# Optimization experiments

Hardware: AMD Instinct MI355X
Metric: run time of the kernel (lower is better)

Reference implementation:

```python
import jax, jax.numpy as jnp
import numpy as np
from jax import lax

DN = ('NCHW', 'OIHW', 'NCHW')


def setup_inputs() -> dict:
    key = jax.random.key(0)
    k_x, k0, k1, k2, k3 = jax.random.split(key, 5)
    return {
        'x': jax.random.normal(k_x, (16, 1, 256, 256), dtype=jnp.float32),
        'w0': jax.random.normal(k0, (16, 1, 25, 25), dtype=jnp.float32) * 0.05,
        'w1': jax.random.normal(k1, (16, 1, 49, 49), dtype=jnp.float32) * 0.02,
        'w2': jax.random.normal(k2, (16, 1, 97, 97), dtype=jnp.float32) * 0.01,
        'w3': jax.random.normal(k3, (16, 1, 193, 193), dtype=jnp.float32) * 0.005,
    }


def _energy(x, w, scale):
    # valid conv -> square -> global average pool, divided by scale. [B, 16]
    y = lax.conv_general_dilated(x, w, window_strides=(1, 1), padding='VALID',
                                 dimension_numbers=DN)
    return jnp.mean(y * y, axis=(2, 3)) / scale


def reference(x, w0, w1, w2, w3):
    feats = [
        _energy(x, w0, 1.0),
        _energy(x, w1, 2.0),
        _energy(x, w2, 4.0),
        _energy(x, w3, 8.0),
    ]
    y = jnp.stack(feats, axis=2)  # [B, 16, 4] == cat of squeezed [B,16,1] along dim 2
    y1, y2 = y[:, :8, :], y[:, 8:, :]  # split(8, dim=1)
    return y1 + y2  # [B, 8, 4]
```

## Files before the change

kernel.cpp:

```cpp
#include <hip/hip_runtime.h>
#include <hip/hip_bf16.h>

typedef __attribute__((ext_vector_type(8))) short short8v;
typedef __attribute__((ext_vector_type(4))) float f32x4;

#define IMG 256
#define NIMG 16
#define XB_ELEMS (NIMG * IMG * IMG)

#define LSTRIDE 768
#define LROWS   32
#define BBUF    (LROWS * LSTRIDE)
#define NI      (BBUF / 1024)

#define WOFF0 0u
#define WOFF1 233472u
#define WOFF2 897024u
#define WOFF3 3010560u
#define WELEMS 9461760u

__global__ void xconvert_kernel(const float* __restrict__ x,
                                __hip_bfloat16* __restrict__ xb) {
  int i = blockIdx.x * blockDim.x + threadIdx.x;
  if (i < XB_ELEMS) xb[i] = __float2bfloat16(x[i]);
}

__global__ void wpack_kernel(const float* __restrict__ w,
                             unsigned short* __restrict__ wp,
                             int K, int NSV, int total) {
  for (int idx = blockIdx.x * blockDim.x + threadIdx.x; idx < total;
       idx += gridDim.x * blockDim.x) {
    int e    = idx & 7;
    int lane = (idx >> 3) & 63;
    int rest = idx >> 9;
    int sv   = rest % NSV; rest /= NSV;
    int up   = rest % (K + 32);
    int sig  = rest / (K + 32);
    int o    = lane & 15;
    int u    = up - 16;
    int v    = sv * 32 + (lane >> 4) * 8 + e - sig;
    float val = (u >= 0 && u < K && v >= 0 && v < K) ? w[(o * K + u) * K + v] : 0.0f;
    __hip_bfloat16 h = __float2bfloat16(val);
    wp[idx] = *(unsigned short*)&h;
  }
}

template <int K, int NSV, int JBA, int WAVES, int HOUT, int IG, unsigned WOFF, int SIDX>
__device__ __forceinline__ void conv_scale(int bl,
                                           const unsigned short* __restrict__ xb,
                                           const unsigned short* __restrict__ wp,
                                           float* __restrict__ E, char* lds) {
  constexpr int RBEND = K + 16;
  constexpr int NCH   = (RBEND + 15) / 16;
  constexpr int TAIL  = RBEND - 16 * (NCH - 1);
  constexpr int M     = (NI + WAVES - 1) / WAVES;
  constexpr int WROW  = NSV * 512;
  constexpr unsigned WSLICE = (unsigned)(K + 32) * WROW;

  const int wv = threadIdx.x >> 6, lane = threadIdx.x & 63;
  const int sig = bl & 7;
  int rest = bl >> 3;
  const int ig = rest % IG, n = rest / IG;
  const int i0 = ig * 32;
  const int lr = lane & 15, lg = lane >> 4;
  const bool act = (wv < WAVES);

  const unsigned short* Wbase = wp + WOFF + (unsigned)sig * WSLICE + (unsigned)lane * 8;
  const unsigned short* Xn = xb + ((unsigned)n << 16);
  unsigned short* lds0 = (unsigned short*)lds;
  unsigned short* lds1 = (unsigned short*)(lds + BBUF);

  auto stage = [&](unsigned short* lb, int chunk) {
#pragma unroll
    for (int k2 = 0; k2 < M; ++k2) {
      int ib = wv + WAVES * k2;
      if (ib >= NI) ib = 0;
      int P = ib * 1024 + lane * 16;
      int row = P / LSTRIDE;
      int col2 = (P - row * LSTRIDE) - ((row & 7) << 4);
      int colE = col2 >> 1;
      if (colE < 0) colE = 0;
      if (colE > 248) colE = 248;
      int grow = i0 + chunk * 16 + row;
      if (grow > 255) grow = 255;
      const unsigned short* gp = Xn + (grow << 8) + colE;
      __builtin_amdgcn_global_load_lds(
          (const __attribute__((address_space(1))) unsigned int*)(const void*)gp,
          (__attribute__((address_space(3))) unsigned int*)(void*)(lb + (P >> 1)),
          16, 0, 0);
    }
  };

  f32x4 acc[2][JBA];
#pragma unroll
  for (int g = 0; g < 2; ++g)
#pragma unroll
    for (int jb = 0; jb < JBA; ++jb) acc[g][jb] = (f32x4)(0.0f);

  if (act) stage(lds0, 0);
  asm volatile("s_waitcnt vmcnt(0)" ::: "memory");
  __builtin_amdgcn_s_barrier();
  __builtin_amdgcn_sched_barrier(0);

  const int cbyte = ((wv * JBA + lg) << 4);

  for (int c = 0; c < NCH; ++c) {
    unsigned short* lb = (c & 1) ? lds1 : lds0;
    if (act) {
      if (c + 1 < NCH) stage((c & 1) ? lds0 : lds1, c + 1);
      const int RL = (c == NCH - 1) ? TAIL : 16;
      const unsigned short* Wc = Wbase + (unsigned)(c * 16) * WROW;
#pragma unroll 2
      for (int rbL = 0; rbL < RL; ++rbL) {
        const int rowLoc = rbL + lr;
        const char* abase = (const char*)lb + rowLoc * LSTRIDE +
                            ((rowLoc & 7) << 4) + cbyte;
        const unsigned short* Wr1 = Wc + rbL * WROW;
        const unsigned short* Wr0 = Wr1 + 16 * WROW;
#pragma unroll
        for (int sv = 0; sv < NSV; ++sv) {
          short8v b0 = *(const short8v*)(Wr0 + sv * 512);
          short8v b1 = *(const short8v*)(Wr1 + sv * 512);
          short8v a_[JBA];
#pragma unroll
          for (int jb = 0; jb < JBA; ++jb)
            a_[jb] = *(const short8v*)(abase + sv * 64 + jb * 16);
#pragma unroll
          for (int jb = 0; jb < JBA; ++jb) {
            acc[0][jb] = __builtin_amdgcn_mfma_f32_16x16x32_bf16(a_[jb], b0, acc[0][jb], 0, 0, 0);
            acc[1][jb] = __builtin_amdgcn_mfma_f32_16x16x32_bf16(a_[jb], b1, acc[1][jb], 0, 0, 0);
          }
        }
      }
    }
    asm volatile("s_waitcnt vmcnt(0)" ::: "memory");
    __builtin_amdgcn_sched_barrier(0);
    __builtin_amdgcn_s_barrier();
    __builtin_amdgcn_sched_barrier(0);
  }

  if (act) {
    float esum = 0.0f;
#pragma unroll
    for (int g = 0; g < 2; ++g)
#pragma unroll
      for (int jb = 0; jb < JBA; ++jb) {
        int j = sig + 8 * (wv * JBA + jb);
#pragma unroll
        for (int r2 = 0; r2 < 4; ++r2) {
          int i = i0 + 16 * g + 4 * lg + r2;
          float v = acc[g][jb][r2];
          esum += (i < HOUT && j < HOUT) ? v * v : 0.0f;
        }
      }
    esum += __shfl_xor(esum, 16, 64);
    esum += __shfl_xor(esum, 32, 64);
    if (lg == 0) atomicAdd(&E[SIDX * 256 + n * 16 + lr], esum);
  }
}

__global__ __launch_bounds__(512, 2) void conv_mfma_kernel(
    const unsigned short* __restrict__ xb, const unsigned short* __restrict__ wp,
    float* __restrict__ E) {
  extern __shared__ char lds[];
  int b = blockIdx.x;
  if (b < 256) {
    conv_scale<193, 7, 2, 4, 64, 2, WOFF3, 3>(b, xb, wp, E, lds);
  } else if (b < 896) {
    conv_scale<97, 4, 4, 5, 160, 5, WOFF2, 2>(b - 256, xb, wp, E, lds);
  } else if (b < 1792) {
    conv_scale<49, 2, 4, 7, 208, 7, WOFF1, 1>(b - 896, xb, wp, E, lds);
  } else {
    conv_scale<25, 1, 4, 8, 232, 8, WOFF0, 0>(b - 1792, xb, wp, E, lds);
  }
}

__global__ void finalize_kernel(const float* __restrict__ E, float* __restrict__ out) {
  int idx = threadIdx.x;
  if (idx >= 512) return;
  int s = idx & 3, c = (idx >> 2) & 7, n = idx >> 5;
  float denom;
  if (s == 0)      denom = 53824.0f;
  else if (s == 1) denom = 86528.0f;
  else if (s == 2) denom = 102400.0f;
  else             denom = 32768.0f;
  out[idx] = (E[s * 256 + n * 16 + c] + E[s * 256 + n * 16 + c + 8]) / denom;
}

extern "C" void kernel_launch(void* const* d_in, const int* in_sizes, int n_in,
                              void* d_out, int out_size, void* d_ws, size_t ws_size,
                              hipStream_t stream) {
  const float* x = (const float*)d_in[0];
  const float* w[4] = {(const float*)d_in[1], (const float*)d_in[2],
                       (const float*)d_in[3], (const float*)d_in[4]};
  static const int Ks[4]   = {25, 49, 97, 193};
  static const int NSVs[4] = {1, 2, 4, 7};
  static const unsigned wOff[4] = {WOFF0, WOFF1, WOFF2, WOFF3};

  char* wsb = (char*)d_ws;
  float* E = (float*)wsb;
  __hip_bfloat16* xb = (__hip_bfloat16*)(wsb + 4096);
  unsigned short* wp = (unsigned short*)(wsb + 4096 + (size_t)XB_ELEMS * 2);

  hipMemsetAsync(E, 0, 1024 * sizeof(float), stream);
  xconvert_kernel<<<(XB_ELEMS + 255) / 256, 256, 0, stream>>>(x, xb);
  for (int s = 0; s < 4; ++s) {
    int total = 8 * (Ks[s] + 32) * NSVs[s] * 512;
    wpack_kernel<<<(total + 255) / 256, 256, 0, stream>>>(w[s], wp + wOff[s],
                                                          Ks[s], NSVs[s], total);
  }
  conv_mfma_kernel<<<2816, 512, 2 * BBUF, stream>>>((const unsigned short*)xb, wp, E);
  finalize_kernel<<<1, 512, 0, stream>>>(E, (float*)d_out);
}
```

Before: 496.9 us.

## Restructure conv tiling: split kernel rows, pair shifts, producer waves, XOR-swizzled LDS

Reorganizes the MFMA convolution. Each block now handles two column shifts at once, so every A fragment read from LDS feeds twice as many MFMAs. The large kernels are split along kernel rows across two blocks. The weight packing drops the 32 rows of zero padding and the two row groups are handled by separate GM-specialized loop bodies, which removes MFMAs on zero weights. LDS shrinks to a 512-byte row stride with an XOR swizzle, occupancy rises to 4 blocks per CU, and when fewer than 8 waves compute, the idle waves act as dedicated producers that stage input tiles. The cost is more atomics, more code paths, and tighter register pressure under the higher occupancy bound.

```diff
diff --git a/kernel.cpp b/kernel.cpp
--- a/kernel.cpp
+++ b/kernel.cpp
@@ -8,16 +8,13 @@
 #define NIMG 16
 #define XB_ELEMS (NIMG * IMG * IMG)
 
-#define LSTRIDE 768
-#define LROWS   32
-#define BBUF    (LROWS * LSTRIDE)
-#define NI      (BBUF / 1024)
-
-#define WOFF0 0u
-#define WOFF1 233472u
-#define WOFF2 897024u
-#define WOFF3 3010560u
-#define WELEMS 9461760u
+#define WQ0 0u
+#define WQ1 102400u
+#define WQ2 503808u
+#define WQ3 2093056u
+#define WQEND 7624704u
+
+#define BUFB 16384
 
 __global__ void xconvert_kernel(const float* __restrict__ x,
                                 __hip_bfloat16* __restrict__ xb) {
@@ -26,152 +23,225 @@
 }
 
 __global__ void wpack_kernel(const float* __restrict__ w,
-                             unsigned short* __restrict__ wp,
+                             unsigned short* __restrict__ wq,
                              int K, int NSV, int total) {
   for (int idx = blockIdx.x * blockDim.x + threadIdx.x; idx < total;
        idx += gridDim.x * blockDim.x) {
-    int e    = idx & 7;
-    int lane = (idx >> 3) & 63;
-    int rest = idx >> 9;
-    int sv   = rest % NSV; rest /= NSV;
-    int up   = rest % (K + 32);
-    int sig  = rest / (K + 32);
-    int o    = lane & 15;
-    int u    = up - 16;
-    int v    = sv * 32 + (lane >> 4) * 8 + e - sig;
-    float val = (u >= 0 && u < K && v >= 0 && v < K) ? w[(o * K + u) * K + v] : 0.0f;
+    int e = idx & 7, lane = (idx >> 3) & 63, rest = idx >> 9;
+    int sv = rest % NSV; rest /= NSV;
+    int u = rest % K, sig = rest / K;
+    int o = lane & 15;
+    int v = sv * 32 + (lane >> 4) * 8 + e - sig;
+    float val = (v >= 0 && v < K) ? w[(o * K + u) * K + v] : 0.0f;
     __hip_bfloat16 h = __float2bfloat16(val);
-    wp[idx] = *(unsigned short*)&h;
-  }
-}
-
-template <int K, int NSV, int JBA, int WAVES, int HOUT, int IG, unsigned WOFF, int SIDX>
-__device__ __forceinline__ void conv_scale(int bl,
-                                           const unsigned short* __restrict__ xb,
-                                           const unsigned short* __restrict__ wp,
-                                           float* __restrict__ E, char* lds) {
-  constexpr int RBEND = K + 16;
-  constexpr int NCH   = (RBEND + 15) / 16;
-  constexpr int TAIL  = RBEND - 16 * (NCH - 1);
-  constexpr int M     = (NI + WAVES - 1) / WAVES;
-  constexpr int WROW  = NSV * 512;
-  constexpr unsigned WSLICE = (unsigned)(K + 32) * WROW;
+    wq[idx] = *(unsigned short*)&h;
+  }
+}
+
+template <int GM, int NSV, int JBA>
+__device__ __forceinline__ void kbody(int c, int rb0, int rb1, const char* bufc,
+                                      const unsigned short* __restrict__ Wa,
+                                      const unsigned short* __restrict__ Wb,
+                                      int cbBase, int lr, f32x4 (&acc)[2][2][JBA]) {
+#pragma unroll 1
+  for (int rbL = rb0; rbL < rb1; ++rbL) {
+    const int rowLoc = rbL + lr;
+    const char* rbase = bufc + rowLoc * 512;
+    const int u0i = 16 * c + rbL;
+#pragma unroll
+    for (int sv = 0; sv < NSV; ++sv) {
+      short8v a_[JBA];
+#pragma unroll
+      for (int jb = 0; jb < JBA; ++jb) {
+        int cb = cbBase + 16 * jb + 64 * sv;
+        int addr = (cb & ~127) + ((((cb >> 4) ^ rowLoc) & 7) << 4);
+        a_[jb] = *(const short8v*)(rbase + addr);
+      }
+      if (GM & 1) {
+        const int wo = (u0i * NSV + sv) * 512;
+        short8v ba = *(const short8v*)(Wa + wo);
+        short8v bb = *(const short8v*)(Wb + wo);
+#pragma unroll
+        for (int jb = 0; jb < JBA; ++jb) {
+          acc[0][0][jb] = __builtin_amdgcn_mfma_f32_16x16x32_bf16(a_[jb], ba, acc[0][0][jb], 0, 0, 0);
+          acc[0][1][jb] = __builtin_amdgcn_mfma_f32_16x16x32_bf16(a_[jb], bb, acc[0][1][jb], 0, 0, 0);
+        }
+      }
+      if (GM & 2) {
+        const int wo = ((u0i - 16) * NSV + sv) * 512;
+        short8v ba = *(const short8v*)(Wa + wo);
+        short8v bb = *(const short8v*)(Wb + wo);
+#pragma unroll
+        for (int jb = 0; jb < JBA; ++jb) {
+          acc[1][0][jb] = __builtin_amdgcn_mfma_f32_16x16x32_bf16(a_[jb], ba, acc[1][0][jb], 0, 0, 0);
+          acc[1][1][jb] = __builtin_amdgcn_mfma_f32_16x16x32_bf16(a_[jb], bb, acc[1][1][jb], 0, 0, 0);
+        }
+      }
+    }
+  }
+}
+
+template <int KL, int KFULL, int NSV, int JBA, int WC, int HOUT, int SIDX>
+__device__ __forceinline__ void conv_scale(const unsigned short* __restrict__ xb,
+                                           const unsigned short* __restrict__ wq_s,
+                                           float* __restrict__ E, char* lds,
+                                           int n, int i0, int u0, int q) {
+  constexpr int M16 = KL >> 4, R = KL & 15;
+  constexpr int NCH = M16 + (R ? 2 : 1);
+  constexpr unsigned SSTRIDE = (unsigned)KFULL * NSV * 512;
 
   const int wv = threadIdx.x >> 6, lane = threadIdx.x & 63;
-  const int sig = bl & 7;
-  int rest = bl >> 3;
-  const int ig = rest % IG, n = rest / IG;
-  const int i0 = ig * 32;
   const int lr = lane & 15, lg = lane >> 4;
-  const bool act = (wv < WAVES);
-
-  const unsigned short* Wbase = wp + WOFF + (unsigned)sig * WSLICE + (unsigned)lane * 8;
+  const bool isProd = (WC < 8) && (wv >= WC);
   const unsigned short* Xn = xb + ((unsigned)n << 16);
-  unsigned short* lds0 = (unsigned short*)lds;
-  unsigned short* lds1 = (unsigned short*)(lds + BBUF);
-
-  auto stage = [&](unsigned short* lb, int chunk) {
+  const int rowG0 = i0 + u0;
+
+  const unsigned short* Wa = wq_s + (unsigned)(2 * q) * SSTRIDE +
+                             (unsigned)(u0 * NSV) * 512 + lane * 8;
+  const unsigned short* Wb = Wa + SSTRIDE;
+
+  auto stage = [&](int cn) {
+    char* dst = lds + (cn & 1) * BUFB;
+    constexpr int NSTG = (WC < 8) ? (8 - WC) : 8;
+    const int sid = (WC < 8) ? (wv - WC) : wv;
+    constexpr int M = (16 + NSTG - 1) / NSTG;
 #pragma unroll
     for (int k2 = 0; k2 < M; ++k2) {
-      int ib = wv + WAVES * k2;
-      if (ib >= NI) ib = 0;
+      int ib = sid + NSTG * k2;
+      if (ib >= 16) ib = 0;
       int P = ib * 1024 + lane * 16;
-      int row = P / LSTRIDE;
-      int col2 = (P - row * LSTRIDE) - ((row & 7) << 4);
-      int colE = col2 >> 1;
-      if (colE < 0) colE = 0;
-      if (colE > 248) colE = 248;
-      int grow = i0 + chunk * 16 + row;
+      int lrow = P >> 9;
+      int slot = (P >> 4) & 31;
+      int srcslot = (slot & ~7) | ((slot ^ lrow) & 7);
+      int grow = rowG0 + cn * 16 + lrow;
       if (grow > 255) grow = 255;
-      const unsigned short* gp = Xn + (grow << 8) + colE;
+      const unsigned short* gp = Xn + (grow << 8) + srcslot * 8;
       __builtin_amdgcn_global_load_lds(
           (const __attribute__((address_space(1))) unsigned int*)(const void*)gp,
-          (__attribute__((address_space(3))) unsigned int*)(void*)(lb + (P >> 1)),
-          16, 0, 0);
+          (__attribute__((address_space(3))) unsigned int*)(void*)(dst + P), 16, 0, 0);
     }
   };
 
-  f32x4 acc[2][JBA];
+  if (isProd) {
+    stage(0);
+    asm volatile("s_waitcnt vmcnt(0)" ::: "memory");
+    __builtin_amdgcn_s_barrier();
+    for (int c = 0; c < NCH; ++c) {
+      if (c + 1 < NCH) {
+        stage(c + 1);
+        asm volatile("s_waitcnt vmcnt(0)" ::: "memory");
+      }
+      __builtin_amdgcn_s_barrier();
+    }
+    return;
+  }
+
+  f32x4 acc[2][2][JBA];
 #pragma unroll
   for (int g = 0; g < 2; ++g)
 #pragma unroll
-    for (int jb = 0; jb < JBA; ++jb) acc[g][jb] = (f32x4)(0.0f);
-
-  if (act) stage(lds0, 0);
-  asm volatile("s_waitcnt vmcnt(0)" ::: "memory");
+    for (int sj = 0; sj < 2; ++sj)
+#pragma unroll
+      for (int jb = 0; jb < JBA; ++jb) acc[g][sj][jb] = (f32x4)(0.0f);
+
+  const int t0 = wv * JBA;
+  const int cbBase = 16 * t0 + 16 * lg;
+
+  if (WC == 8) {
+    stage(0);
+    asm volatile("s_waitcnt vmcnt(0)" ::: "memory");
+  }
   __builtin_amdgcn_s_barrier();
-  __builtin_amdgcn_sched_barrier(0);
-
-  const int cbyte = ((wv * JBA + lg) << 4);
-
-  for (int c = 0; c < NCH; ++c) {
-    unsigned short* lb = (c & 1) ? lds1 : lds0;
-    if (act) {
-      if (c + 1 < NCH) stage((c & 1) ? lds0 : lds1, c + 1);
-      const int RL = (c == NCH - 1) ? TAIL : 16;
-      const unsigned short* Wc = Wbase + (unsigned)(c * 16) * WROW;
-#pragma unroll 2
-      for (int rbL = 0; rbL < RL; ++rbL) {
-        const int rowLoc = rbL + lr;
-        const char* abase = (const char*)lb + rowLoc * LSTRIDE +
-                            ((rowLoc & 7) << 4) + cbyte;
-        const unsigned short* Wr1 = Wc + rbL * WROW;
-        const unsigned short* Wr0 = Wr1 + 16 * WROW;
-#pragma unroll
-        for (int sv = 0; sv < NSV; ++sv) {
-          short8v b0 = *(const short8v*)(Wr0 + sv * 512);
-          short8v b1 = *(const short8v*)(Wr1 + sv * 512);
-          short8v a_[JBA];
-#pragma unroll
-          for (int jb = 0; jb < JBA; ++jb)
-            a_[jb] = *(const short8v*)(abase + sv * 64 + jb * 16);
-#pragma unroll
-          for (int jb = 0; jb < JBA; ++jb) {
-            acc[0][jb] = __builtin_amdgcn_mfma_f32_16x16x32_bf16(a_[jb], b0, acc[0][jb], 0, 0, 0);
-            acc[1][jb] = __builtin_amdgcn_mfma_f32_16x16x32_bf16(a_[jb], b1, acc[1][jb], 0, 0, 0);
-          }
-        }
-      }
-    }
-    asm volatile("s_waitcnt vmcnt(0)" ::: "memory");
-    __builtin_amdgcn_sched_barrier(0);
-    __builtin_amdgcn_s_barrier();
-    __builtin_amdgcn_sched_barrier(0);
-  }
-
-  if (act) {
-    float esum = 0.0f;
-#pragma unroll
-    for (int g = 0; g < 2; ++g)
+
+#define STEP_PRE(c)  if (WC == 8 && (c) + 1 < NCH) stage((c) + 1);
+#define STEP_POST()  if (WC == 8) asm volatile("s_waitcnt vmcnt(0)" ::: "memory"); \
+                     __builtin_amdgcn_s_barrier();
+
+  {
+    const char* bufc = lds;
+    STEP_PRE(0)
+    kbody<1, NSV, JBA>(0, 0, 16, bufc, Wa, Wb, cbBase, lr, acc);
+    STEP_POST()
+  }
+#pragma unroll 1
+  for (int c = 1; c < M16; ++c) {
+    const char* bufc = lds + (c & 1) * BUFB;
+    STEP_PRE(c)
+    kbody<3, NSV, JBA>(c, 0, 16, bufc, Wa, Wb, cbBase, lr, acc);
+    STEP_POST()
+  }
+  if (R > 0) {
+    {
+      const char* bufc = lds + (M16 & 1) * BUFB;
+      STEP_PRE(M16)
+      kbody<3, NSV, JBA>(M16, 0, R, bufc, Wa, Wb, cbBase, lr, acc);
+      kbody<2, NSV, JBA>(M16, R, 16, bufc, Wa, Wb, cbBase, lr, acc);
+      STEP_POST()
+    }
+    {
+      const char* bufc = lds + ((M16 + 1) & 1) * BUFB;
+      kbody<2, NSV, JBA>(M16 + 1, 0, R, bufc, Wa, Wb, cbBase, lr, acc);
+      STEP_POST()
+    }
+  } else {
+    const char* bufc = lds + (M16 & 1) * BUFB;
+    kbody<2, NSV, JBA>(M16, 0, 16, bufc, Wa, Wb, cbBase, lr, acc);
+    STEP_POST()
+  }
+#undef STEP_PRE
+#undef STEP_POST
+
+  float esum = 0.0f;
+#pragma unroll
+  for (int g = 0; g < 2; ++g)
+#pragma unroll
+    for (int sj = 0; sj < 2; ++sj)
 #pragma unroll
       for (int jb = 0; jb < JBA; ++jb) {
-        int j = sig + 8 * (wv * JBA + jb);
+        int j = 8 * (t0 + jb) + 2 * q + sj;
 #pragma unroll
         for (int r2 = 0; r2 < 4; ++r2) {
           int i = i0 + 16 * g + 4 * lg + r2;
-          float v = acc[g][jb][r2];
+          float v = acc[g][sj][jb][r2];
           esum += (i < HOUT && j < HOUT) ? v * v : 0.0f;
         }
       }
-    esum += __shfl_xor(esum, 16, 64);
-    esum += __shfl_xor(esum, 32, 64);
-    if (lg == 0) atomicAdd(&E[SIDX * 256 + n * 16 + lr], esum);
-  }
-}
-
-__global__ __launch_bounds__(512, 2) void conv_mfma_kernel(
-    const unsigned short* __restrict__ xb, const unsigned short* __restrict__ wp,
+  esum += __shfl_xor(esum, 16, 64);
+  esum += __shfl_xor(esum, 32, 64);
+  if (lg == 0) atomicAdd(&E[SIDX * 256 + n * 16 + lr], esum);
+}
+
+__global__ __launch_bounds__(512, 4) void conv_mfma_kernel(
+    const unsigned short* __restrict__ xb, const unsigned short* __restrict__ wq,
     float* __restrict__ E) {
-  extern __shared__ char lds[];
+  __shared__ char lds[2 * BUFB];
   int b = blockIdx.x;
   if (b < 256) {
-    conv_scale<193, 7, 2, 4, 64, 2, WOFF3, 3>(b, xb, wp, E, lds);
+    int q = (b & 7) >> 1;
+    int rest = ((b >> 3) << 1) | (b & 1);
+    int ks = rest & 1, ig = (rest >> 1) & 1, n = rest >> 2;
+    if (ks == 0) conv_scale<96, 193, 7, 2, 4, 64, 3>(xb, wq + WQ3, E, lds, n, ig * 32, 0, q);
+    else         conv_scale<97, 193, 7, 2, 4, 64, 3>(xb, wq + WQ3, E, lds, n, ig * 32, 96, q);
   } else if (b < 896) {
-    conv_scale<97, 4, 4, 5, 160, 5, WOFF2, 2>(b - 256, xb, wp, E, lds);
-  } else if (b < 1792) {
-    conv_scale<49, 2, 4, 7, 208, 7, WOFF1, 1>(b - 896, xb, wp, E, lds);
+    int bl = b - 256;
+    int q = (bl & 7) >> 1;
+    int rest = ((bl >> 3) << 1) | (bl & 1);
+    int ks = rest & 1, r2 = rest >> 1;
+    int ig = r2 % 5, n = r2 / 5;
+    if (ks == 0) conv_scale<48, 97, 4, 4, 5, 160, 2>(xb, wq + WQ2, E, lds, n, ig * 32, 0, q);
+    else         conv_scale<49, 97, 4, 4, 5, 160, 2>(xb, wq + WQ2, E, lds, n, ig * 32, 48, q);
+  } else if (b < 1344) {
+    int bl = b - 896;
+    int q = (bl & 7) >> 1;
+    int rest = ((bl >> 3) << 1) | (bl & 1);
+    int ig = rest % 7, n = rest / 7;
+    conv_scale<49, 49, 2, 4, 7, 208, 1>(xb, wq + WQ1, E, lds, n, ig * 32, 0, q);
   } else {
-    conv_scale<25, 1, 4, 8, 232, 8, WOFF0, 0>(b - 1792, xb, wp, E, lds);
+    int bl = b - 1344;
+    int q = (bl & 7) >> 1;
+    int rest = ((bl >> 3) << 1) | (bl & 1);
+    int ig = rest & 7, n = rest >> 3;
+    conv_scale<25, 25, 1, 4, 8, 232, 0>(xb, wq + WQ0, E, lds, n, ig * 32, 0, q);
   }
 }
 
@@ -193,22 +263,21 @@
   const float* x = (const float*)d_in[0];
   const float* w[4] = {(const float*)d_in[1], (const float*)d_in[2],
                        (const float*)d_in[3], (const float*)d_in[4]};
-  static const int Ks[4]   = {25, 49, 97, 193};
+  static const int Ks[4] = {25, 49, 97, 193};
   static const int NSVs[4] = {1, 2, 4, 7};
-  static const unsigned wOff[4] = {WOFF0, WOFF1, WOFF2, WOFF3};
+  static const unsigned wOff[4] = {WQ0, WQ1, WQ2, WQ3};
 
   char* wsb = (char*)d_ws;
   float* E = (float*)wsb;
   __hip_bfloat16* xb = (__hip_bfloat16*)(wsb + 4096);
-  unsigned short* wp = (unsigned short*)(wsb + 4096 + (size_t)XB_ELEMS * 2);
+  unsigned short* wq = (unsigned short*)(wsb + 4096 + (size_t)XB_ELEMS * 2);
 
   hipMemsetAsync(E, 0, 1024 * sizeof(float), stream);
   xconvert_kernel<<<(XB_ELEMS + 255) / 256, 256, 0, stream>>>(x, xb);
   for (int s = 0; s < 4; ++s) {
-    int total = 8 * (Ks[s] + 32) * NSVs[s] * 512;
-    wpack_kernel<<<(total + 255) / 256, 256, 0, stream>>>(w[s], wp + wOff[s],
-                                                          Ks[s], NSVs[s], total);
-  }
-  conv_mfma_kernel<<<2816, 512, 2 * BBUF, stream>>>((const unsigned short*)xb, wp, E);
+    int total = 8 * Ks[s] * NSVs[s] * 512;
+    wpack_kernel<<<2048, 256, 0, stream>>>(w[s], wq + wOff[s], Ks[s], NSVs[s], total);
+  }
+  conv_mfma_kernel<<<1856, 512, 0, stream>>>((const unsigned short*)xb, wq, E);
   finalize_kernel<<<1, 512, 0, stream>>>(E, (float*)d_out);
 }
```

Measured after the change: 587.4 us. 1.18x slower.
